# Kernel optimization log

Measured on AMD Instinct MI355X. Metric: run time of the kernel, lower is better.

## Reference

```python
import jax, jax.numpy as jnp
import numpy as np

B, C, H, W = 4, 16, 512, 512


def setup_inputs() -> dict:
    key = jax.random.key(0)
    k1, k2, k3, k4, k5 = jax.random.split(key, 5)
    # positive depth in [0.5, 10.5] meters
    depth = jax.random.uniform(k1, (B, 1, H, W), dtype=jnp.float32) * 10.0 + 0.5
    # realistic, well-conditioned camera intrinsics per batch element
    fx = 500.0 + 20.0 * jax.random.normal(k2, (B,), dtype=jnp.float32)
    fy = 500.0 + 20.0 * jax.random.normal(k3, (B,), dtype=jnp.float32)
    zeros = jnp.zeros((B,), jnp.float32)
    ones = jnp.ones((B,), jnp.float32)
    K = jnp.stack([
        jnp.stack([fx, zeros, ones * (W / 2.0)], axis=-1),
        jnp.stack([zeros, fy, ones * (H / 2.0)], axis=-1),
        jnp.stack([zeros, zeros, ones], axis=-1),
    ], axis=1)  # [B,3,3]
    # near-identity rigid-ish transforms so homogeneous w ~ 1
    T = jnp.eye(4, dtype=jnp.float32)[None, None] + 0.05 * jax.random.normal(k4, (B, C, 4, 4), dtype=jnp.float32)
    masks = jax.random.randint(k5, (B, C, H, W), 0, 2).astype(jnp.bool_)
    return {"depth": depth, "K": K, "T": T, "masks": masks}


def reference(depth, K, T, masks):
    b, _, h, w = depth.shape
    c = masks.shape[1]
    n = h * w
    eps = 1e-10
    # --- depth -> point cloud ---
    u = jnp.arange(w, dtype=depth.dtype)
    v = jnp.arange(h, dtype=depth.dtype)
    uu, vv = jnp.meshgrid(u, v, indexing='xy')            # [H,W]
    uv1 = jnp.stack([uu, vv, jnp.ones_like(uu)], axis=-1)  # [H,W,3]
    K_inv = jnp.linalg.inv(K)                              # [B,3,3]
    d = jnp.transpose(depth, (0, 2, 3, 1))                 # [B,H,W,1]
    points_3d = jnp.einsum('bij,hwj->bhwi', K_inv, uv1) * d  # [B,H,W,3]
    # --- per-object masked transform (vectorized over all channels) ---
    pts = points_3d.reshape(b, n, 3)
    pts_h = jnp.concatenate([pts, jnp.ones((b, n, 1), pts.dtype)], axis=-1)  # [B,N,4]
    trans_h = jnp.einsum('bcij,bnj->bcni', T, pts_h)       # [B,C,N,4]
    trans3 = trans_h[..., :3] / (trans_h[..., 3:] + eps)   # [B,C,N,3]
    masks_flat = masks.reshape(b, c, n)
    out = pts
    for ci in range(c):
        out = jnp.where(masks_flat[:, ci, :, None], trans3[:, ci], out)
    tp = out.reshape(b, h, w, 3)                           # transformed points
    # --- reproject to depth map (scatter) ---
    p2h = jnp.einsum('bij,bhwj->bhwi', K, tp)              # [B,H,W,3]
    p2 = p2h[..., :2] / (p2h[..., 2:] + eps)
    Z = tp[..., 2]                                         # [B,H,W]
    u_idx = jnp.clip(p2[..., 0], 0, w - 1).astype(jnp.int32)
    v_idx = jnp.clip(p2[..., 1], 0, h - 1).astype(jnp.int32)
    b_idx = jnp.broadcast_to(jnp.arange(b)[:, None, None], (b, h, w))
    depth_map = depth.at[b_idx, 0, v_idx, u_idx].set(Z)
    return depth_map
```

## Files before the change

### kernel.cpp

```cpp
#include <hip/hip_runtime.h>
#include <stdint.h>

constexpr int B = 4, C = 16, H = 512, W = 512;
constexpr int N = H * W;
constexpr float EPS = 1e-10f;

__global__ __launch_bounds__(256) void project_scatter_kernel(
    const float* __restrict__ depth,
    const float* __restrict__ K,
    const float* __restrict__ T,
    const int*   __restrict__ masks,
    unsigned long long* __restrict__ ws)
{
    int idx = blockIdx.x * blockDim.x + threadIdx.x;
    if (idx >= B * N) return;
    int b = idx / N;
    int n = idx - b * N;
    int v = n / W;
    int u = n - v * W;

    float d = depth[idx];

    const float* Kb = K + b * 9;
    float k00 = Kb[0], k01 = Kb[1], k02 = Kb[2];
    float k10 = Kb[3], k11 = Kb[4], k12 = Kb[5];
    float k20 = Kb[6], k21 = Kb[7], k22 = Kb[8];

    float c00 =  (k11 * k22 - k12 * k21);
    float c01 = -(k10 * k22 - k12 * k20);
    float c02 =  (k10 * k21 - k11 * k20);
    float det = k00 * c00 + k01 * c01 + k02 * c02;
    float invdet = 1.0f / det;
    float i00 =  (k11 * k22 - k12 * k21) * invdet;
    float i01 = -(k01 * k22 - k02 * k21) * invdet;
    float i02 =  (k01 * k12 - k02 * k11) * invdet;
    float i10 = -(k10 * k22 - k12 * k20) * invdet;
    float i11 =  (k00 * k22 - k02 * k20) * invdet;
    float i12 = -(k00 * k12 - k02 * k10) * invdet;
    float i20 =  (k10 * k21 - k11 * k20) * invdet;
    float i21 = -(k00 * k21 - k01 * k20) * invdet;
    float i22 =  (k00 * k11 - k01 * k10) * invdet;

    float uf = (float)u, vf = (float)v;
    float px = (i00 * uf + i01 * vf + i02) * d;
    float py = (i10 * uf + i11 * vf + i12) * d;
    float pz = (i20 * uf + i21 * vf + i22) * d;

    float ox = px, oy = py, oz = pz;
    const int* mb = masks + (size_t)b * C * N + n;
    for (int c = C - 1; c >= 0; --c) {
        if (mb[(size_t)c * N] != 0) {
            const float* Tm = T + ((size_t)b * C + c) * 16;
            float tx = Tm[0]  * px + Tm[1]  * py + Tm[2]  * pz + Tm[3];
            float ty = Tm[4]  * px + Tm[5]  * py + Tm[6]  * pz + Tm[7];
            float tz = Tm[8]  * px + Tm[9]  * py + Tm[10] * pz + Tm[11];
            float tw = Tm[12] * px + Tm[13] * py + Tm[14] * pz + Tm[15];
            float denom = tw + EPS;
            ox = tx / denom;
            oy = ty / denom;
            oz = tz / denom;
            break;
        }
    }

    float qx = k00 * ox + k01 * oy + k02 * oz;
    float qy = k10 * ox + k11 * oy + k12 * oz;
    float qz = k20 * ox + k21 * oy + k22 * oz;
    float zz = qz + EPS;
    float pu = qx / zz;
    float pv = qy / zz;
    pu = fminf(fmaxf(pu, 0.0f), (float)(W - 1));
    pv = fminf(fmaxf(pv, 0.0f), (float)(H - 1));
    int ui = (int)pu;
    int vi = (int)pv;

    float Z = oz;
    unsigned long long key =
        ((unsigned long long)(unsigned)(n + 1) << 32) |
        (unsigned long long)__float_as_uint(Z);
    atomicMax(&ws[(size_t)b * N + (size_t)vi * W + ui], key);
}

__global__ __launch_bounds__(256) void resolve_kernel(
    const unsigned long long* __restrict__ ws,
    const float* __restrict__ depth,
    float* __restrict__ out)
{
    int idx = blockIdx.x * blockDim.x + threadIdx.x;
    if (idx >= B * N) return;
    unsigned long long key = ws[idx];
    out[idx] = (key >> 32) ? __uint_as_float((unsigned)key) : depth[idx];
}

extern "C" void kernel_launch(void* const* d_in, const int* in_sizes, int n_in,
                              void* d_out, int out_size, void* d_ws, size_t ws_size,
                              hipStream_t stream) {
    const float* depth = (const float*)d_in[0];
    const float* K     = (const float*)d_in[1];
    const float* T     = (const float*)d_in[2];
    const int*   masks = (const int*)d_in[3];
    float* out = (float*)d_out;

    unsigned long long* keys = (unsigned long long*)d_ws;

    hipMemsetAsync(keys, 0, (size_t)B * N * sizeof(unsigned long long), stream);

    int total = B * N;
    int block = 256;
    int grid = (total + block - 1) / block;
    project_scatter_kernel<<<grid, block, 0, stream>>>(depth, K, T, masks, keys);
    resolve_kernel<<<grid, block, 0, stream>>>(keys, depth, out);
}
```

Baseline: 142.6 us.

## Use 32-bit index atomics with side z-buffer and batch mask loads

Measured after the change: 141.4 us. Within noise of the previous version (-0.9%).

```diff
diff --git a/kernel.cpp b/kernel.cpp
--- a/kernel.cpp
+++ b/kernel.cpp
@@ -3,6 +3,7 @@
 
 constexpr int B = 4, C = 16, H = 512, W = 512;
 constexpr int N = H * W;
+constexpr int BLOCKS_PER_BATCH = N / 256;
 constexpr float EPS = 1e-10f;
 
 __global__ __launch_bounds__(256) void project_scatter_kernel(
@@ -10,14 +11,14 @@
     const float* __restrict__ K,
     const float* __restrict__ T,
     const int*   __restrict__ masks,
-    unsigned long long* __restrict__ ws)
+    unsigned*    __restrict__ keys,
+    float*       __restrict__ zbuf)
 {
-    int idx = blockIdx.x * blockDim.x + threadIdx.x;
-    if (idx >= B * N) return;
-    int b = idx / N;
-    int n = idx - b * N;
-    int v = n / W;
-    int u = n - v * W;
+    int b = blockIdx.x >> 10;
+    int n = ((blockIdx.x & (BLOCKS_PER_BATCH - 1)) << 8) + threadIdx.x;
+    int idx = b * N + n;
+    int v = n >> 9;
+    int u = n & (W - 1);
 
     float d = depth[idx];
 
@@ -46,21 +47,32 @@
     float py = (i10 * uf + i11 * vf + i12) * d;
     float pz = (i20 * uf + i21 * vf + i22) * d;
 
+    const int* mb = masks + (size_t)b * C * N + n;
+    int sel = -1;
+    #pragma unroll
+    for (int g = 3; g >= 0; --g) {
+        int m3 = mb[(size_t)(4 * g + 3) * N];
+        int m2 = mb[(size_t)(4 * g + 2) * N];
+        int m1 = mb[(size_t)(4 * g + 1) * N];
+        int m0 = mb[(size_t)(4 * g + 0) * N];
+        int s = (m3 != 0) ? (4 * g + 3)
+              : (m2 != 0) ? (4 * g + 2)
+              : (m1 != 0) ? (4 * g + 1)
+              : (m0 != 0) ? (4 * g + 0) : -1;
+        if (s >= 0) { sel = s; break; }
+    }
+
     float ox = px, oy = py, oz = pz;
-    const int* mb = masks + (size_t)b * C * N + n;
-    for (int c = C - 1; c >= 0; --c) {
-        if (mb[(size_t)c * N] != 0) {
-            const float* Tm = T + ((size_t)b * C + c) * 16;
-            float tx = Tm[0]  * px + Tm[1]  * py + Tm[2]  * pz + Tm[3];
-            float ty = Tm[4]  * px + Tm[5]  * py + Tm[6]  * pz + Tm[7];
-            float tz = Tm[8]  * px + Tm[9]  * py + Tm[10] * pz + Tm[11];
-            float tw = Tm[12] * px + Tm[13] * py + Tm[14] * pz + Tm[15];
-            float denom = tw + EPS;
-            ox = tx / denom;
-            oy = ty / denom;
-            oz = tz / denom;
-            break;
-        }
+    if (sel >= 0) {
+        const float* Tm = T + ((size_t)b * C + sel) * 16;
+        float tx = Tm[0]  * px + Tm[1]  * py + Tm[2]  * pz + Tm[3];
+        float ty = Tm[4]  * px + Tm[5]  * py + Tm[6]  * pz + Tm[7];
+        float tz = Tm[8]  * px + Tm[9]  * py + Tm[10] * pz + Tm[11];
+        float tw = Tm[12] * px + Tm[13] * py + Tm[14] * pz + Tm[15];
+        float denom = tw + EPS;
+        ox = tx / denom;
+        oy = ty / denom;
+        oz = tz / denom;
     }
 
     float qx = k00 * ox + k01 * oy + k02 * oz;
@@ -74,22 +86,21 @@
     int ui = (int)pu;
     int vi = (int)pv;
 
-    float Z = oz;
-    unsigned long long key =
-        ((unsigned long long)(unsigned)(n + 1) << 32) |
-        (unsigned long long)__float_as_uint(Z);
-    atomicMax(&ws[(size_t)b * N + (size_t)vi * W + ui], key);
+    zbuf[idx] = oz;
+    atomicMax(&keys[(size_t)b * N + (size_t)vi * W + ui], (unsigned)(n + 1));
 }
 
 __global__ __launch_bounds__(256) void resolve_kernel(
-    const unsigned long long* __restrict__ ws,
-    const float* __restrict__ depth,
-    float* __restrict__ out)
+    const unsigned* __restrict__ keys,
+    const float*    __restrict__ zbuf,
+    const float*    __restrict__ depth,
+    float*          __restrict__ out)
 {
-    int idx = blockIdx.x * blockDim.x + threadIdx.x;
-    if (idx >= B * N) return;
-    unsigned long long key = ws[idx];
-    out[idx] = (key >> 32) ? __uint_as_float((unsigned)key) : depth[idx];
+    int b = blockIdx.x >> 10;
+    int n = ((blockIdx.x & (BLOCKS_PER_BATCH - 1)) << 8) + threadIdx.x;
+    int idx = b * N + n;
+    unsigned k = keys[idx];
+    out[idx] = k ? zbuf[(size_t)b * N + (k - 1)] : depth[idx];
 }
 
 extern "C" void kernel_launch(void* const* d_in, const int* in_sizes, int n_in,
@@ -101,13 +112,12 @@
     const int*   masks = (const int*)d_in[3];
     float* out = (float*)d_out;
 
-    unsigned long long* keys = (unsigned long long*)d_ws;
+    unsigned* keys = (unsigned*)d_ws;
+    float*    zbuf = (float*)((char*)d_ws + (size_t)B * N * sizeof(unsigned));
 
-    hipMemsetAsync(keys, 0, (size_t)B * N * sizeof(unsigned long long), stream);
+    hipMemsetAsync(keys, 0, (size_t)B * N * sizeof(unsigned), stream);
 
-    int total = B * N;
-    int block = 256;
-    int grid = (total + block - 1) / block;
-    project_scatter_kernel<<<grid, block, 0, stream>>>(depth, K, T, masks, keys);
-    resolve_kernel<<<grid, block, 0, stream>>>(keys, depth, out);
+    int grid = B * BLOCKS_PER_BATCH;
+    project_scatter_kernel<<<grid, 256, 0, stream>>>(depth, K, T, masks, keys, zbuf);
+    resolve_kernel<<<grid, 256, 0, stream>>>(keys, zbuf, depth, out);
 }
```
